# Kernel optimization log

Measured on AMD Instinct MI355X. Metric: run time of the kernel, lower is better.

The kernel has to match this reference:

```python
import jax, jax.numpy as jnp
import numpy as np

D_MODEL = 1024
H = 16
D_K = D_MODEL // H


def setup_inputs() -> dict:
    key = jax.random.key(0)
    ks = jax.random.split(key, 12)
    B, S = 4, 2048
    s = 1.0 / np.sqrt(D_MODEL)
    return {
        "Q": jax.random.normal(ks[0], (B, S, D_MODEL), jnp.float32),
        "K": jax.random.normal(ks[1], (B, S, D_MODEL), jnp.float32),
        "V": jax.random.normal(ks[2], (B, S, D_MODEL), jnp.float32),
        "attn_mask": jnp.ones((B, S), jnp.int32),
        "Wq": jax.random.normal(ks[3], (D_MODEL, D_MODEL), jnp.float32) * s,
        "bq": jax.random.normal(ks[4], (D_MODEL,), jnp.float32) * s,
        "Wk": jax.random.normal(ks[5], (D_MODEL, D_MODEL), jnp.float32) * s,
        "bk": jax.random.normal(ks[6], (D_MODEL,), jnp.float32) * s,
        "Wv": jax.random.normal(ks[7], (D_MODEL, D_MODEL), jnp.float32) * s,
        "bv": jax.random.normal(ks[8], (D_MODEL,), jnp.float32) * s,
        "Wo": jax.random.normal(ks[9], (D_MODEL, D_MODEL), jnp.float32) * s,
        "bo": jax.random.normal(ks[10], (D_MODEL,), jnp.float32) * s,
    }


def _split_heads(x):
    B, S, _ = x.shape
    return x.reshape(B, S, H, D_K).transpose(0, 2, 1, 3)  # (B,H,S,Dk)


def reference(Q, K, V, attn_mask, Wq, bq, Wk, bk, Wv, bv, Wo, bo):
    # Linear projections (torch Linear: x @ W.T + b)
    q = _split_heads(Q @ Wq.T + bq)
    k = _split_heads(K @ Wk.T + bk)
    v = _split_heads(V @ Wv.T + bv)
    scale = 1.0 / jnp.sqrt(jnp.asarray(D_K, q.dtype))
    scores = jnp.einsum("bhqd,bhkd->bhqk", q, k) * scale  # (B,H,S,S)
    # 2-D mask (B,S) broadcast over heads and query positions; 0 -> -inf
    mask = attn_mask[:, None, None, :]
    scores = jnp.where(mask == 0, -jnp.inf, scores)
    attn = jax.nn.softmax(scores, axis=-1)
    # dropout_proba = 0.0 -> identity
    x = jnp.einsum("bhqk,bhkd->bhqd", attn, v)
    B, _, S, _ = x.shape
    x = x.transpose(0, 2, 1, 3).reshape(B, S, D_MODEL)
    return x @ Wo.T + bo
```

## Files before the change

### kernel.cpp

```cpp
#include <hip/hip_runtime.h>
#include <stdint.h>

typedef unsigned short u16;
typedef __attribute__((ext_vector_type(8))) unsigned short u16x8;
typedef __attribute__((ext_vector_type(4))) unsigned short u16x4;
typedef __attribute__((ext_vector_type(2))) __fp16 h16x2;
typedef __attribute__((ext_vector_type(4))) _Float16 f16x4;
typedef __attribute__((ext_vector_type(8))) _Float16 f16x8;
typedef __attribute__((ext_vector_type(4))) float f32x4;

#define MFMA16F16(a,b,c)  __builtin_amdgcn_mfma_f32_16x16x16f16((a),(b),(c),0,0,0)
#define MFMA32F16(a,b,c)  __builtin_amdgcn_mfma_f32_16x16x32_f16((a),(b),(c),0,0,0)

__device__ __forceinline__ f32x4 f4zero() {
    f32x4 z; z[0]=0.f; z[1]=0.f; z[2]=0.f; z[3]=0.f; return z;
}
__device__ __forceinline__ u16x8 cvth8(float4 a, float4 b) {
    union { h16x2 h[4]; u16x8 u; } U;
    U.h[0] = __builtin_amdgcn_cvt_pkrtz(a.x, a.y);
    U.h[1] = __builtin_amdgcn_cvt_pkrtz(a.z, a.w);
    U.h[2] = __builtin_amdgcn_cvt_pkrtz(b.x, b.y);
    U.h[3] = __builtin_amdgcn_cvt_pkrtz(b.z, b.w);
    return U.u;
}

#define GLDS(gp, lp) __builtin_amdgcn_global_load_lds( \
    (const __attribute__((address_space(1))) void*)(gp), \
    (__attribute__((address_space(3))) void*)(lp), 16, 0, 0)

#define QSC 0.1803368801111601f

__global__ __launch_bounds__(256) void conv_w(
    const float* __restrict__ w0, const float* __restrict__ w1,
    const float* __restrict__ w2, const float* __restrict__ w3,
    u16* __restrict__ out)
{
    const int t = blockIdx.x >> 8;
    const float* src = (t == 0) ? w0 : (t == 1) ? w1 : (t == 2) ? w2 : w3;
    const size_t idx = (size_t)(blockIdx.x & 255) * 4096 + (size_t)threadIdx.x * 16;
    u16* dst = out + (size_t)t * 1048576 + idx;
    float4 a0 = *(const float4*)(src + idx);
    float4 a1 = *(const float4*)(src + idx + 4);
    float4 a2 = *(const float4*)(src + idx + 8);
    float4 a3 = *(const float4*)(src + idx + 12);
    *(u16x8*)dst       = cvth8(a0, a1);
    *(u16x8*)(dst + 8) = cvth8(a2, a3);
}

template<int MODE>
__global__ __launch_bounds__(256, 3) void gemm_qkv(
    const float* __restrict__ Qf, const float* __restrict__ Kf, const float* __restrict__ Vf,
    const u16* __restrict__ wc,
    const float* __restrict__ Wqf, const float* __restrict__ Wkf, const float* __restrict__ Wvf,
    const float* __restrict__ bq, const float* __restrict__ bk, const float* __restrict__ bv,
    u16* __restrict__ qhp, u16* __restrict__ khp, u16* __restrict__ vtp)
{
    __shared__ __align__(16) u16 smem[24576];
    u16* Ct = smem;

    const int t  = blockIdx.y >> 3;
    const int n0 = (blockIdx.y & 7) * 128;
    const int m0 = blockIdx.x * 128;
    const float* X    = (t == 0) ? Qf : (t == 1) ? Kf : Vf;
    const float* Wf   = (t == 0) ? Wqf : (t == 1) ? Wkf : Wvf;
    const float* bias = (t == 0) ? bq : (t == 1) ? bk : bv;
    const u16*   Wb   = wc + (size_t)t * 1048576;
    u16*         dst  = (t == 0) ? qhp : (t == 1) ? khp : vtp;
    const float  scl  = (t == 0) ? QSC : 1.0f;

    const int tid  = threadIdx.x;
    const int wave = tid >> 6, lane = tid & 63;
    const int quad = lane >> 4, l16 = lane & 15;
    const int wm = (wave >> 1) * 64, wn = (wave & 1) * 64;

    const int srow = lane >> 2;
    const size_t scol = (size_t)(lane & 3) * 8;
    const int sr = tid >> 1, hh = tid & 1;

    f32x4 acc[4][4];
    for (int i = 0; i < 4; i++) for (int j = 0; j < 4; j++) acc[i][j] = f4zero();

    auto stageB = [&](int b, int kt) {
        GLDS(Wb + (size_t)(n0 + wave * 32 +      srow) * 1024 + kt * 32 + scol,
             smem + b * 8192 + 4096 + wave * 1024);
        GLDS(Wb + (size_t)(n0 + wave * 32 + 16 + srow) * 1024 + kt * 32 + scol,
             smem + b * 8192 + 4096 + wave * 1024 + 512);
    };
    float4 xr_[4];
    auto loadX = [&](int kt) {
        const float* p = X + (size_t)(m0 + sr) * 1024 + kt * 32 + hh * 16;
        xr_[0] = *(const float4*)(p);     xr_[1] = *(const float4*)(p + 4);
        xr_[2] = *(const float4*)(p + 8); xr_[3] = *(const float4*)(p + 12);
    };
    auto writeX = [&](int b) {
        u16* d = smem + b * 8192 + sr * 32 + hh * 16;
        *(u16x8*)d       = cvth8(xr_[0], xr_[1]);
        *(u16x8*)(d + 8) = cvth8(xr_[2], xr_[3]);
    };
    auto comp = [&](int b) {
        const u16* As = smem + b * 8192;
        const u16* Bs = As + 4096;
        f16x8 af[4], bfr[4];
#pragma unroll
        for (int i = 0; i < 4; i++) {
            af[i]  = *(const f16x8*)(As + (wm + i * 16 + l16) * 32 + quad * 8);
            bfr[i] = *(const f16x8*)(Bs + (wn + i * 16 + l16) * 32 + quad * 8);
        }
        __builtin_amdgcn_s_setprio(1);
#pragma unroll
        for (int i = 0; i < 4; i++)
#pragma unroll
            for (int j = 0; j < 4; j++)
                acc[i][j] = MFMA32F16(af[i], bfr[j], acc[i][j]);
        __builtin_amdgcn_s_setprio(0);
    };

    if (MODE == 0) {
        for (int kt = 0; kt < 32; ++kt) {
            loadX(kt); writeX(0);
            const float* p = Wf + (size_t)(n0 + sr) * 1024 + kt * 32 + hh * 16;
            float4 b0 = *(const float4*)(p);     float4 b1 = *(const float4*)(p + 4);
            float4 b2 = *(const float4*)(p + 8); float4 b3 = *(const float4*)(p + 12);
            u16* d = smem + 4096 + sr * 32 + hh * 16;
            *(u16x8*)d       = cvth8(b0, b1);
            *(u16x8*)(d + 8) = cvth8(b2, b3);
            __syncthreads();
            comp(0);
            __syncthreads();
        }
    } else {
        stageB(0, 0);
        stageB(1, 1);
        loadX(0); writeX(0);
        int bA = 0, bB = 1, bC = 2;
        for (int kt = 0; kt < 31; ++kt) {
            asm volatile("s_waitcnt vmcnt(2) lgkmcnt(0)" ::: "memory");
            __builtin_amdgcn_s_barrier();
            __builtin_amdgcn_sched_barrier(0);
            loadX(kt + 1);
            if (kt < 30) stageB(bC, kt + 2);
            comp(bA);
            writeX(bB);
            int tmp = bA; bA = bB; bB = bC; bC = tmp;
        }
        asm volatile("s_waitcnt vmcnt(0) lgkmcnt(0)" ::: "memory");
        __builtin_amdgcn_s_barrier();
        __builtin_amdgcn_sched_barrier(0);
        comp(bA);
    }
    __syncthreads();

#pragma unroll
    for (int i = 0; i < 4; i++) {
        const int row = wm + i * 16 + quad * 4;
#pragma unroll
        for (int j = 0; j < 4; j++) {
            const int col = wn + j * 16 + l16;
            const float bv2 = bias[n0 + col];
#pragma unroll
            for (int r = 0; r < 2; r++) {
                union { h16x2 h; unsigned u; } P;
                P.h = __builtin_amdgcn_cvt_pkrtz((acc[i][j][2*r] + bv2) * scl,
                                                 (acc[i][j][2*r+1] + bv2) * scl);
                Ct[(row + 2*r)     * 136 + col] = (u16)(P.u & 0xFFFF);
                Ct[(row + 2*r + 1) * 136 + col] = (u16)(P.u >> 16);
            }
        }
    }
    __syncthreads();

    if (t < 2) {
        const int row = tid >> 1, half = tid & 1;
        const int m = m0 + row, b = m >> 11, s = m & 2047;
        const int h = (n0 >> 6) + half;
        u16* o = dst + ((size_t)(b * 16 + h) * 2048 + s) * 64;
        const u16* src = Ct + row * 136 + half * 64;
#pragma unroll
        for (int j = 0; j < 64; j += 8) *(u16x8*)(o + j) = *(const u16x8*)(src + j);
    } else {
        const int col = tid >> 1, shalf = tid & 1;
        const int h = (n0 >> 6) + (col >> 6), d = col & 63;
        const int mb = m0 + shalf * 64, b = mb >> 11, sb = mb & 2047;
        u16* o = dst + (size_t)((b * 16 + h) * 64 + d) * 2048 + sb;
#pragma unroll
        for (int j0 = 0; j0 < 64; j0 += 8) {
            u16x8 tv;
#pragma unroll
            for (int j = 0; j < 8; j++) tv[j] = Ct[(shalf * 64 + j0 + j) * 136 + col];
            *(u16x8*)(o + j0) = tv;
        }
    }
}

template<int MODE>
__global__ __launch_bounds__(256, 3) void gemm_o(
    const u16* __restrict__ Xb, const u16* __restrict__ wcO,
    const float* __restrict__ Wf, const float* __restrict__ bias,
    float* __restrict__ out)
{
    __shared__ __align__(16) u16 smem[24576];

    const int tid  = threadIdx.x;
    const int wave = tid >> 6, lane = tid & 63;
    const int quad = lane >> 4, l16 = lane & 15;
    const int m0 = blockIdx.x * 128, n0 = blockIdx.y * 128;
    const int wm = (wave >> 1) * 64, wn = (wave & 1) * 64;

    const int srow = lane >> 2;
    const size_t scol = (size_t)(lane & 3) * 8;
    const int sr = tid >> 1, hh = tid & 1;

    f32x4 acc[4][4];
    for (int i = 0; i < 4; i++) for (int j = 0; j < 4; j++) acc[i][j] = f4zero();

    auto stageA = [&](int b, int kt) {
        GLDS(Xb + (size_t)(m0 + wave * 32 +      srow) * 1024 + kt * 32 + scol,
             smem + b * 8192 + wave * 1024);
        GLDS(Xb + (size_t)(m0 + wave * 32 + 16 + srow) * 1024 + kt * 32 + scol,
             smem + b * 8192 + wave * 1024 + 512);
    };
    auto stageB = [&](int b, int kt) {
        GLDS(wcO + (size_t)(n0 + wave * 32 +      srow) * 1024 + kt * 32 + scol,
             smem + b * 8192 + 4096 + wave * 1024);
        GLDS(wcO + (size_t)(n0 + wave * 32 + 16 + srow) * 1024 + kt * 32 + scol,
             smem + b * 8192 + 4096 + wave * 1024 + 512);
    };
    float4 wr_[4];
    auto loadW = [&](int kt) {
        const float* p = Wf + (size_t)(n0 + sr) * 1024 + kt * 32 + hh * 16;
        wr_[0] = *(const float4*)(p);     wr_[1] = *(const float4*)(p + 4);
        wr_[2] = *(const float4*)(p + 8); wr_[3] = *(const float4*)(p + 12);
    };
    auto writeW = [&](int b) {
        u16* d = smem + b * 8192 + 4096 + sr * 32 + hh * 16;
        *(u16x8*)d       = cvth8(wr_[0], wr_[1]);
        *(u16x8*)(d + 8) = cvth8(wr_[2], wr_[3]);
    };
    auto comp = [&](int b) {
        const u16* As = smem + b * 8192;
        const u16* Bs = As + 4096;
        f16x8 af[4], bfr[4];
#pragma unroll
        for (int i = 0; i < 4; i++) {
            af[i]  = *(const f16x8*)(As + (wm + i * 16 + l16) * 32 + quad * 8);
            bfr[i] = *(const f16x8*)(Bs + (wn + i * 16 + l16) * 32 + quad * 8);
        }
        __builtin_amdgcn_s_setprio(1);
#pragma unroll
        for (int i = 0; i < 4; i++)
#pragma unroll
            for (int j = 0; j < 4; j++)
                acc[i][j] = MFMA32F16(af[i], bfr[j], acc[i][j]);
        __builtin_amdgcn_s_setprio(0);
    };

    stageA(0, 0);
    if (MODE == 2) stageB(0, 0);
    stageA(1, 1);
    if (MODE == 2) stageB(1, 1);
    if (MODE == 1) { loadW(0); writeW(0); }
    int bA = 0, bB = 1, bC = 2;
    for (int kt = 0; kt < 31; ++kt) {
        if (MODE == 2) asm volatile("s_waitcnt vmcnt(4) lgkmcnt(0)" ::: "memory");
        else           asm volatile("s_waitcnt vmcnt(2) lgkmcnt(0)" ::: "memory");
        __builtin_amdgcn_s_barrier();
        __builtin_amdgcn_sched_barrier(0);
        if (MODE == 1) loadW(kt + 1);
        if (kt < 30) {
            stageA(bC, kt + 2);
            if (MODE == 2) stageB(bC, kt + 2);
        }
        comp(bA);
        if (MODE == 1) writeW(bB);
        int tmp = bA; bA = bB; bB = bC; bC = tmp;
    }
    asm volatile("s_waitcnt vmcnt(0) lgkmcnt(0)" ::: "memory");
    __builtin_amdgcn_s_barrier();
    __builtin_amdgcn_sched_barrier(0);
    comp(bA);

#pragma unroll
    for (int i = 0; i < 4; i++)
#pragma unroll
        for (int j = 0; j < 4; j++) {
            const int col = wn + j * 16 + l16;
            const float bv = bias[n0 + col];
#pragma unroll
            for (int r = 0; r < 4; r++)
                out[(size_t)(m0 + wm + i * 16 + quad * 4 + r) * 1024 + n0 + col] = acc[i][j][r] + bv;
        }
}

__global__ __launch_bounds__(256, 4) void attn_fused(
    const u16* __restrict__ qh, const u16* __restrict__ kh,
    const u16* __restrict__ vth, const int* __restrict__ mask,
    u16* __restrict__ xout)
{
    __shared__ __align__(16) u16 Ksh[2][4096];
    __shared__ __align__(16) u16 Vsh[2][4352];
    __shared__ float mshf[2][64];

    const int tid = threadIdx.x, wave = tid >> 6, lane = tid & 63;
    const int quad = lane >> 4, l16 = lane & 15;

    const int flat = blockIdx.x + (blockIdx.y << 4);
    const int xr = flat & 7, xc_ = flat >> 3;
    const int qb = xc_ & 15, bh = xr + ((xc_ >> 4) << 3);
    const int b = bh >> 4, h = bh & 15;
    const int wq = qb * 128 + wave * 32;

    f16x8 qf[2][2];
#pragma unroll
    for (int qg = 0; qg < 2; qg++)
#pragma unroll
        for (int kc = 0; kc < 2; kc++)
            qf[qg][kc] = *(const f16x8*)(qh + ((size_t)bh * 2048 + wq + qg * 16 + l16) * 64
                                         + kc * 32 + quad * 8);

    f32x4 o[2][4];
#pragma unroll
    for (int qg = 0; qg < 2; qg++)
        for (int dt = 0; dt < 4; dt++) o[qg][dt] = f4zero();
    f32x4 lacc[2]; lacc[0] = f4zero(); lacc[1] = f4zero();
    f16x4 ones;
    ones[0] = (_Float16)1.f; ones[1] = (_Float16)1.f;
    ones[2] = (_Float16)1.f; ones[3] = (_Float16)1.f;

    const int klr = lane >> 3;
    const size_t kgoff = (size_t)((lane & 7) ^ klr) << 3;
    const u16* kgb = kh + (size_t)bh * 2048 * 64;

    const int skey = tid >> 2, sc = (tid & 3) * 16;
    const u16* vg = vth + ((size_t)bh * 64 + skey) * 2048 + sc;
    const int mrow = b * 2048;

    {
        GLDS(kgb + (size_t)(wave * 16 + klr) * 64 + kgoff,     &Ksh[0][wave * 1024]);
        GLDS(kgb + (size_t)(wave * 16 + 8 + klr) * 64 + kgoff, &Ksh[0][wave * 1024 + 512]);
        const u16x8 v0 = *(const u16x8*)(vg);
        const u16x8 v1 = *(const u16x8*)(vg + 8);
        u16* vd = &Vsh[0][skey * 68 + sc];
        *(u16x4*)(vd)      = (u16x4){v0[0], v0[1], v0[2], v0[3]};
        *(u16x4*)(vd + 4)  = (u16x4){v0[4], v0[5], v0[6], v0[7]};
        *(u16x4*)(vd + 8)  = (u16x4){v1[0], v1[1], v1[2], v1[3]};
        *(u16x4*)(vd + 12) = (u16x4){v1[4], v1[5], v1[6], v1[7]};
        if (tid < 64) mshf[0][tid] = mask[mrow + tid] ? -10.0f : -1.0e30f;
    }
    __syncthreads();

    for (int t = 0; t < 32; ++t) {
        const int cur = t & 1;
        const u16* Kc = &Ksh[cur][0];
        const u16* Vc = &Vsh[cur][0];

        u16x8 v0, v1; int mreg = 1;
        const int kk2 = (t + 1) * 64;
        if (t < 31) {
            GLDS(kgb + (size_t)(kk2 + wave * 16 + klr) * 64 + kgoff,
                 &Ksh[cur ^ 1][wave * 1024]);
            GLDS(kgb + (size_t)(kk2 + wave * 16 + 8 + klr) * 64 + kgoff,
                 &Ksh[cur ^ 1][wave * 1024 + 512]);
            v0 = *(const u16x8*)(vg + kk2);
            v1 = *(const u16x8*)(vg + kk2 + 8);
            if (tid < 64) mreg = mask[mrow + kk2 + tid];
        }

        __builtin_amdgcn_s_setprio(1);
        f16x4 pf[4][2];
#pragma unroll
        for (int nt = 0; nt < 4; nt++) {
            const int kro = (nt * 16 + l16) * 64;
            const f16x8 kf0 = *(const f16x8*)(Kc + kro + ((quad ^ (l16 & 7)) << 3));
            const f16x8 kf1 = *(const f16x8*)(Kc + kro + (((quad ^ 4) ^ (l16 & 7)) << 3));
            const float4 mb = *(const float4*)(&mshf[cur][nt * 16 + quad * 4]);
#pragma unroll
            for (int qg = 0; qg < 2; qg++) {
                f32x4 z;
                z[0] = mb.x; z[1] = mb.y; z[2] = mb.z; z[3] = mb.w;
                z = MFMA32F16(kf0, qf[qg][0], z);
                z = MFMA32F16(kf1, qf[qg][1], z);
                union { h16x2 h[2]; f16x4 v; } U;
                U.h[0] = __builtin_amdgcn_cvt_pkrtz(__builtin_amdgcn_exp2f(z[0]),
                                                    __builtin_amdgcn_exp2f(z[1]));
                U.h[1] = __builtin_amdgcn_cvt_pkrtz(__builtin_amdgcn_exp2f(z[2]),
                                                    __builtin_amdgcn_exp2f(z[3]));
                pf[nt][qg] = U.v;
            }
        }
#pragma unroll
        for (int nt = 0; nt < 4; nt++) {
            lacc[0] = MFMA16F16(ones, pf[nt][0], lacc[0]);
            lacc[1] = MFMA16F16(ones, pf[nt][1], lacc[1]);
        }
#pragma unroll
        for (int dt = 0; dt < 4; dt++) {
#pragma unroll
            for (int nt = 0; nt < 4; nt++) {
                const f16x4 vf = *(const f16x4*)(Vc + (dt * 16 + l16) * 68 + nt * 16 + quad * 4);
                o[0][dt] = MFMA16F16(vf, pf[nt][0], o[0][dt]);
                o[1][dt] = MFMA16F16(vf, pf[nt][1], o[1][dt]);
            }
        }
        __builtin_amdgcn_s_setprio(0);

        if (t < 31) {
            u16* vd = &Vsh[cur ^ 1][skey * 68 + sc];
            *(u16x4*)(vd)      = (u16x4){v0[0], v0[1], v0[2], v0[3]};
            *(u16x4*)(vd + 4)  = (u16x4){v0[4], v0[5], v0[6], v0[7]};
            *(u16x4*)(vd + 8)  = (u16x4){v1[0], v1[1], v1[2], v1[3]};
            *(u16x4*)(vd + 12) = (u16x4){v1[4], v1[5], v1[6], v1[7]};
            if (tid < 64) mshf[cur ^ 1][tid] = mreg ? -10.0f : -1.0e30f;
        }
        __syncthreads();
    }

#pragma unroll
    for (int qg = 0; qg < 2; qg++) {
        const float inv = 1.0f / lacc[qg][0];
        const int row = wq + qg * 16 + l16;
        u16* op = xout + ((size_t)b * 2048 + row) * 1024 + h * 64;
#pragma unroll
        for (int dt = 0; dt < 4; dt++) {
            union { h16x2 h[2]; u16x4 u; } U;
            U.h[0] = __builtin_amdgcn_cvt_pkrtz(o[qg][dt][0] * inv, o[qg][dt][1] * inv);
            U.h[1] = __builtin_amdgcn_cvt_pkrtz(o[qg][dt][2] * inv, o[qg][dt][3] * inv);
            *(u16x4*)(op + dt * 16 + quad * 4) = U.u;
        }
    }
}

extern "C" void kernel_launch(void* const* d_in, const int* in_sizes, int n_in,
                              void* d_out, int out_size, void* d_ws, size_t ws_size,
                              hipStream_t stream)
{
    const float* Q   = (const float*)d_in[0];
    const float* K   = (const float*)d_in[1];
    const float* V   = (const float*)d_in[2];
    const int*   msk = (const int*)d_in[3];
    const float* Wq  = (const float*)d_in[4];
    const float* bq  = (const float*)d_in[5];
    const float* Wk  = (const float*)d_in[6];
    const float* bk  = (const float*)d_in[7];
    const float* Wv  = (const float*)d_in[8];
    const float* bv  = (const float*)d_in[9];
    const float* Wo  = (const float*)d_in[10];
    const float* bo  = (const float*)d_in[11];

    u16* base = (u16*)d_ws;
    dim3 blk(256);
    dim3 gq(64, 24);
    dim3 ga(16, 64);
    dim3 go(64, 8);

    if (ws_size >= ((size_t)72 << 20)) {
        u16* wc  = base;
        u16* qhp = base + 4194304;
        u16* khp = qhp + 8388608;
        u16* vtp = khp + 8388608;
        u16* xs  = vtp + 8388608;
        conv_w<<<1024, blk, 0, stream>>>(Wq, Wk, Wv, Wo, wc);
        gemm_qkv<1><<<gq, blk, 0, stream>>>(Q, K, V, wc,
            nullptr, nullptr, nullptr, bq, bk, bv, qhp, khp, vtp);
        attn_fused<<<ga, blk, 0, stream>>>(qhp, khp, vtp, msk, xs);
        gemm_o<2><<<go, blk, 0, stream>>>(xs, wc + 3 * 1048576, nullptr, bo, (float*)d_out);
    } else {
        u16* qhp = base;
        u16* khp = qhp + 8388608;
        u16* vtp = khp + 8388608;
        u16* xs  = vtp + 8388608;
        gemm_qkv<0><<<gq, blk, 0, stream>>>(Q, K, V, nullptr,
            Wq, Wk, Wv, bq, bk, bv, qhp, khp, vtp);
        attn_fused<<<ga, blk, 0, stream>>>(qhp, khp, vtp, msk, xs);
        gemm_o<1><<<go, blk, 0, stream>>>(xs, nullptr, Wo, bo, (float*)d_out);
    }
}
```

Before: 362.0 us.

## Deepen X prefetch to two stages with coalesced row mapping in QKV projection

Changes the fp32 X tile loads in the projection GEMM to use four threads per row with 8-float chunks over two 64-row halves, which improves coalescing. Two alternating register sets (A/B) now keep X loads two k-steps ahead, and the loop is unrolled by two with a raised vmcnt wait threshold. This hides global load latency behind more MFMA work. It costs extra registers, which could reduce occupancy, and the waitcnt accounting is harder to get right.

```diff
diff --git a/kernel.cpp b/kernel.cpp
--- a/kernel.cpp
+++ b/kernel.cpp
@@ -75,6 +75,9 @@
 
     const int srow = lane >> 2;
     const size_t scol = (size_t)(lane & 3) * 8;
+    const int sr2 = tid >> 2, c2 = tid & 3;
+    const float* Xb1 = X + (size_t)(m0 + sr2) * 1024 + c2 * 8;
+    const float* Xb2 = Xb1 + (size_t)64 * 1024;
     const int sr = tid >> 1, hh = tid & 1;
 
     f32x4 acc[4][4];
@@ -86,16 +89,24 @@
         GLDS(Wb + (size_t)(n0 + wave * 32 + 16 + srow) * 1024 + kt * 32 + scol,
              smem + b * 8192 + 4096 + wave * 1024 + 512);
     };
-    float4 xr_[4];
-    auto loadX = [&](int kt) {
-        const float* p = X + (size_t)(m0 + sr) * 1024 + kt * 32 + hh * 16;
-        xr_[0] = *(const float4*)(p);     xr_[1] = *(const float4*)(p + 4);
-        xr_[2] = *(const float4*)(p + 8); xr_[3] = *(const float4*)(p + 12);
-    };
-    auto writeX = [&](int b) {
-        u16* d = smem + b * 8192 + sr * 32 + hh * 16;
-        *(u16x8*)d       = cvth8(xr_[0], xr_[1]);
-        *(u16x8*)(d + 8) = cvth8(xr_[2], xr_[3]);
+    float4 xa_[4], xb_[4];
+    auto loadXA = [&](int kt) {
+        xa_[0] = *(const float4*)(Xb1 + kt * 32);     xa_[1] = *(const float4*)(Xb1 + kt * 32 + 4);
+        xa_[2] = *(const float4*)(Xb2 + kt * 32);     xa_[3] = *(const float4*)(Xb2 + kt * 32 + 4);
+    };
+    auto loadXB = [&](int kt) {
+        xb_[0] = *(const float4*)(Xb1 + kt * 32);     xb_[1] = *(const float4*)(Xb1 + kt * 32 + 4);
+        xb_[2] = *(const float4*)(Xb2 + kt * 32);     xb_[3] = *(const float4*)(Xb2 + kt * 32 + 4);
+    };
+    auto writeXA = [&](int b) {
+        u16* d = smem + b * 8192 + sr2 * 32 + c2 * 8;
+        *(u16x8*)d          = cvth8(xa_[0], xa_[1]);
+        *(u16x8*)(d + 2048) = cvth8(xa_[2], xa_[3]);
+    };
+    auto writeXB = [&](int b) {
+        u16* d = smem + b * 8192 + sr2 * 32 + c2 * 8;
+        *(u16x8*)d          = cvth8(xb_[0], xb_[1]);
+        *(u16x8*)(d + 2048) = cvth8(xb_[2], xb_[3]);
     };
     auto comp = [&](int b) {
         const u16* As = smem + b * 8192;
@@ -117,7 +128,7 @@
 
     if (MODE == 0) {
         for (int kt = 0; kt < 32; ++kt) {
-            loadX(kt); writeX(0);
+            loadXA(kt); writeXA(0);
             const float* p = Wf + (size_t)(n0 + sr) * 1024 + kt * 32 + hh * 16;
             float4 b0 = *(const float4*)(p);     float4 b1 = *(const float4*)(p + 4);
             float4 b2 = *(const float4*)(p + 8); float4 b3 = *(const float4*)(p + 12);
@@ -131,18 +142,36 @@
     } else {
         stageB(0, 0);
         stageB(1, 1);
-        loadX(0); writeX(0);
+        loadXA(0); writeXA(0);
+        loadXB(1);
         int bA = 0, bB = 1, bC = 2;
-        for (int kt = 0; kt < 31; ++kt) {
-            asm volatile("s_waitcnt vmcnt(2) lgkmcnt(0)" ::: "memory");
+        for (int kt = 0; kt < 30; kt += 2) {
+            asm volatile("s_waitcnt vmcnt(6) lgkmcnt(0)" ::: "memory");
             __builtin_amdgcn_s_barrier();
             __builtin_amdgcn_sched_barrier(0);
-            loadX(kt + 1);
-            if (kt < 30) stageB(bC, kt + 2);
+            loadXA(kt + 2);
+            stageB(bC, kt + 2);
             comp(bA);
-            writeX(bB);
-            int tmp = bA; bA = bB; bB = bC; bC = tmp;
-        }
+            __builtin_amdgcn_sched_barrier(0);
+            writeXB(bB);
+            { int tmp = bA; bA = bB; bB = bC; bC = tmp; }
+            asm volatile("s_waitcnt vmcnt(6) lgkmcnt(0)" ::: "memory");
+            __builtin_amdgcn_s_barrier();
+            __builtin_amdgcn_sched_barrier(0);
+            loadXB(kt + 3);
+            stageB(bC, kt + 3);
+            comp(bA);
+            __builtin_amdgcn_sched_barrier(0);
+            writeXA(bB);
+            { int tmp = bA; bA = bB; bB = bC; bC = tmp; }
+        }
+        asm volatile("s_waitcnt vmcnt(6) lgkmcnt(0)" ::: "memory");
+        __builtin_amdgcn_s_barrier();
+        __builtin_amdgcn_sched_barrier(0);
+        comp(bA);
+        __builtin_amdgcn_sched_barrier(0);
+        writeXB(bB);
+        { int tmp = bA; bA = bB; bB = bC; bC = tmp; }
         asm volatile("s_waitcnt vmcnt(0) lgkmcnt(0)" ::: "memory");
         __builtin_amdgcn_s_barrier();
         __builtin_amdgcn_sched_barrier(0);
```

Result: faster. 345.9 us (-4.4%).
